# Optimization experiments

Measured on AMD Instinct MI355X. Metric: run time of the kernel, lower is better.

Reference implementation:

```python
import jax, jax.numpy as jnp
import numpy as np

BIG = 1e30  # stand-in for +inf that keeps gradients finite


def setup_inputs() -> dict:
    key = jax.random.key(0)
    B, D, N = 32, 128, 2048
    kx, ky, kl = jax.random.split(key, 3)
    x = jax.random.normal(kx, (B, D, N), dtype=jnp.float32)
    y = jax.random.normal(ky, (B, D, N), dtype=jnp.float32)
    # ragged cardinalities in [N//2, N]; every set nonempty
    lens = jax.random.randint(kl, (B,), N // 2, N + 1)
    mask = jnp.arange(N)[None, :] < lens[:, None]  # [B, N] bool
    return {"x": x, "y": y, "mask": mask}


def reference(x, y, mask):
    # x, y: [B, D, N]; mask: [B, N] bool (shared between x and y, as in original)
    xt = jnp.transpose(x, (0, 2, 1))  # [B, N, D]
    yt = jnp.transpose(y, (0, 2, 1))  # [B, N, D]
    x2 = jnp.sum(xt * xt, axis=-1)    # [B, N]
    y2 = jnp.sum(yt * yt, axis=-1)    # [B, N]
    # pairwise squared L2: [B, N, N], d[b,i,j] = ||x_i - y_j||^2
    d = x2[:, :, None] + y2[:, None, :] - 2.0 * jnp.einsum("bid,bjd->bij", xt, yt)
    m = mask
    # x_dist: for each valid y_j, min over valid x_i; then sum over valid j
    d_row = jnp.where(m[:, :, None], d, BIG)              # mask invalid i
    x_dist = jnp.sum(jnp.where(m, jnp.min(d_row, axis=1), 0.0), axis=1)  # [B]
    # y_dist: for each valid x_i, min over valid y_j; then sum over valid i
    d_col = jnp.where(m[:, None, :], d, BIG)              # mask invalid j
    y_dist = jnp.sum(jnp.where(m, jnp.min(d_col, axis=2), 0.0), axis=1)  # [B]
    return jnp.mean(x_dist + y_dist)
```

## Files before the change

kernel.cpp:

```cpp
#include <hip/hip_runtime.h>
#include <hip/hip_bf16.h>

#define BATCH 32
#define DIM   128
#define NPTS  2048
#define NCH   16
#define BIGF  1e30f

#define OFF_XT   0ull
#define OFF_YT   16777216ull
#define OFF_XN   33554432ull
#define OFF_YN   (OFF_XN + 262144ull)
#define OFF_RMIN (OFF_XN + 2ull * 262144ull)
#define OFF_CMIN (OFF_XN + 3ull * 262144ull)

typedef __bf16 bf16x8 __attribute__((ext_vector_type(8)));
typedef float  f32x16 __attribute__((ext_vector_type(16)));

#define ZERO16 {0.f,0.f,0.f,0.f,0.f,0.f,0.f,0.f,0.f,0.f,0.f,0.f,0.f,0.f,0.f,0.f}

__device__ __forceinline__ bool mask_is_i32(const void* m) {
  return ((const unsigned char*)m)[1] == 0;
}
__device__ __forceinline__ bool mask_at(const void* m, bool i32, int idx) {
  return i32 ? (((const int*)m)[idx] != 0) : (((const unsigned char*)m)[idx] != 0);
}

__global__ void chamfer_prep(const float* __restrict__ x, const float* __restrict__ y,
                             const void* __restrict__ mask, char* __restrict__ ws,
                             float* __restrict__ out) {
  __shared__ float buf[128 * 132];
  __shared__ float nrm_part[2][128];

  int blk = blockIdx.x;
  int arr = blk >> 9;
  int b   = (blk >> 4) & 31;
  int nt  = blk & 15;
  int n0  = nt << 7;
  int tid = threadIdx.x;
  bool i32m = mask_is_i32(mask);

  if (blk == 0 && tid == 0) out[0] = 0.f;

  float*    nrm  = (float*)(ws + (arr ? OFF_YN : OFF_XN));
  unsigned* cmin = (unsigned*)(ws + OFF_CMIN);

  if (!mask_at(mask, i32m, b * NPTS + n0)) {
    if (tid < 128) {
      nrm[b * NPTS + n0 + tid] = BIGF;
      if (arr) cmin[b * NPTS + n0 + tid] = __float_as_uint(BIGF);
    }
    return;
  }

  const float* src = (arr ? y : x) + (size_t)b * DIM * NPTS;
#pragma unroll
  for (int k = 0; k < 16; ++k) {
    int idx = k * 256 + tid;
    int d = idx >> 5, c4 = idx & 31;
    *(float4*)&buf[d * 132 + c4 * 4] =
        *(const float4*)(src + (size_t)d * NPTS + n0 + c4 * 4);
  }
  __syncthreads();

  int n = tid & 127, half = tid >> 7;
  char* imgbase = ws + (arr ? OFF_YT : OFF_XT);
  float sq = 0.f;
#pragma unroll
  for (int cl = 0; cl < 8; ++cl) {
    unsigned short h[8];
#pragma unroll
    for (int q = 0; q < 8; ++q) {
      float v = buf[(half * 64 + cl * 8 + q) * 132 + n];
      __hip_bfloat16 bv = __float2bfloat16(v);
      h[q] = *(unsigned short*)&bv;
      float vb = __bfloat162float(bv);
      sq = fmaf(vb, vb, sq);
    }
    uint4 pk;
    pk.x = h[0] | ((unsigned)h[1] << 16);
    pk.y = h[2] | ((unsigned)h[3] << 16);
    pk.z = h[4] | ((unsigned)h[5] << 16);
    pk.w = h[6] | ((unsigned)h[7] << 16);
    int cg = half * 8 + cl;
    *(uint4*)(imgbase + (((size_t)(b * NCH + cg) * NPTS + n0 + n) << 4)) = pk;
  }
  nrm_part[half][n] = sq;
  __syncthreads();
  if (half == 0) {
    float tot = nrm_part[0][n] + nrm_part[1][n];
    int row = n0 + n;
    bool valid = mask_at(mask, i32m, b * NPTS + row);
    nrm[b * NPTS + row] = valid ? tot : BIGF;
    if (arr) cmin[b * NPTS + row] = __float_as_uint(BIGF);
  }
}

__global__ __launch_bounds__(512, 2)
void chamfer_dist(char* __restrict__ ws, const void* __restrict__ mask) {
  __shared__ __align__(16) char ysl[2][NCH * 128 * 16];
  __shared__ unsigned colmin_lds[NPTS];
  __shared__ int lred[8];

  int blk = blockIdx.x;
  int b  = blk & 31;
  int it = blk >> 5;
  int i0 = it << 8;
  int tid = threadIdx.x, lane = tid & 63, w = tid >> 6;
  int qrow = w >> 1, qcol = w & 1, la31 = lane & 31, la5 = lane >> 5;

  bool i32m = mask_is_i32(mask);
  int cnt = 0;
#pragma unroll
  for (int k = 0; k < 4; ++k)
    cnt += mask_at(mask, i32m, b * NPTS + k * 512 + tid) ? 1 : 0;
#pragma unroll
  for (int s = 1; s < 64; s <<= 1) cnt += __shfl_xor(cnt, s);
  if (lane == 0) lred[w] = cnt;
  __syncthreads();
  int len = 0;
#pragma unroll
  for (int k = 0; k < 8; ++k) len += lred[k];
  if (i0 >= len) return;

  const char* xTb = ws + OFF_XT + ((size_t)b * NCH * NPTS << 4);
  const char* yTb = ws + OFF_YT + ((size_t)b * NCH * NPTS << 4);
  const float* xng = (const float*)(ws + OFF_XN) + b * NPTS;
  const float* yng = (const float*)(ws + OFF_YN) + b * NPTS;
  float*    rowming = (float*)(ws + OFF_RMIN) + b * NPTS;
  unsigned* colming = (unsigned*)(ws + OFF_CMIN) + b * NPTS;

#pragma unroll
  for (int k = 0; k < 4; ++k)
    colmin_lds[k * 512 + tid] = __float_as_uint(BIGF);

  int r0 = i0 + qrow * 64 + la31;
  bf16x8 Areg0[8], Areg1[8];
#pragma unroll
  for (int kc = 0; kc < 8; ++kc) {
    int c = kc * 2 + la5;
    Areg0[kc] = *(const bf16x8*)(xTb + (((size_t)c * NPTS + r0) << 4));
    Areg1[kc] = *(const bf16x8*)(xTb + (((size_t)c * NPTS + r0 + 32) << 4));
  }

  float xnr[2][16], rmin[2][16];
#pragma unroll
  for (int fm = 0; fm < 2; ++fm)
#pragma unroll
    for (int r = 0; r < 16; ++r) {
      int row = qrow * 64 + fm * 32 + (r & 3) + ((r >> 2) << 3) + (la5 << 2);
      xnr[fm][r] = xng[i0 + row];
      rmin[fm][r] = BIGF;
    }

  int nT = (len + 127) >> 7;

#pragma unroll
  for (int k = 0; k < 4; ++k) {
    int idx = k * 512 + tid;
    *(uint4*)(ysl[0] + idx * 16) =
        *(const uint4*)(yTb + (((size_t)(idx >> 7) * NPTS + (idx & 127)) << 4));
  }
  __syncthreads();

  for (int jt = 0; jt < nT; ++jt) {
    int cur = jt & 1;
    uint4 stg0, stg1, stg2, stg3;
    if (jt + 1 < nT) {
      int j0n = (jt + 1) << 7;
      int i0d = tid, i1d = 512 + tid, i2d = 1024 + tid, i3d = 1536 + tid;
      stg0 = *(const uint4*)(yTb + (((size_t)(i0d >> 7) * NPTS + j0n + (i0d & 127)) << 4));
      stg1 = *(const uint4*)(yTb + (((size_t)(i1d >> 7) * NPTS + j0n + (i1d & 127)) << 4));
      stg2 = *(const uint4*)(yTb + (((size_t)(i2d >> 7) * NPTS + j0n + (i2d & 127)) << 4));
      stg3 = *(const uint4*)(yTb + (((size_t)(i3d >> 7) * NPTS + j0n + (i3d & 127)) << 4));
    }
    int j0t = (jt << 7) + qcol * 64;
    float ynr0 = yng[j0t + la31];
    float ynr1 = yng[j0t + 32 + la31];

    const char* ybuf = (const char*)ysl[cur];
    f32x16 acc00 = ZERO16, acc01 = ZERO16, acc10 = ZERO16, acc11 = ZERO16;
#pragma unroll
    for (int kc = 0; kc < 8; ++kc) {
      int boff = ((kc * 2 + la5) * 128 + qcol * 64 + la31) << 4;
      bf16x8 b0 = *(const bf16x8*)(ybuf + boff);
      bf16x8 b1 = *(const bf16x8*)(ybuf + boff + (32 << 4));
      acc00 = __builtin_amdgcn_mfma_f32_32x32x16_bf16(Areg0[kc], b0, acc00, 0, 0, 0);
      acc01 = __builtin_amdgcn_mfma_f32_32x32x16_bf16(Areg0[kc], b1, acc01, 0, 0, 0);
      acc10 = __builtin_amdgcn_mfma_f32_32x32x16_bf16(Areg1[kc], b0, acc10, 0, 0, 0);
      acc11 = __builtin_amdgcn_mfma_f32_32x32x16_bf16(Areg1[kc], b1, acc11, 0, 0, 0);
    }
    float cm0 = BIGF, cm1 = BIGF;
#pragma unroll
    for (int r = 0; r < 16; ++r) {
      float u00 = fmaf(-2.f, acc00[r], ynr0);
      float u01 = fmaf(-2.f, acc01[r], ynr1);
      float u10 = fmaf(-2.f, acc10[r], ynr0);
      float u11 = fmaf(-2.f, acc11[r], ynr1);
      rmin[0][r] = fminf(rmin[0][r], fminf(u00, u01));
      rmin[1][r] = fminf(rmin[1][r], fminf(u10, u11));
      cm0 = fminf(cm0, fminf(u00 + xnr[0][r], u10 + xnr[1][r]));
      cm1 = fminf(cm1, fminf(u01 + xnr[0][r], u11 + xnr[1][r]));
    }
    cm0 = fminf(cm0, __shfl_xor(cm0, 32));
    cm1 = fminf(cm1, __shfl_xor(cm1, 32));
    if (lane < 32) {
      atomicMin(&colmin_lds[j0t + la31],      __float_as_uint(fmaxf(cm0, 0.f)));
      atomicMin(&colmin_lds[j0t + 32 + la31], __float_as_uint(fmaxf(cm1, 0.f)));
    }
    if (jt + 1 < nT) {
      char* dst = (char*)ysl[cur ^ 1];
      *(uint4*)(dst + (size_t)(tid)        * 16) = stg0;
      *(uint4*)(dst + (size_t)(512  + tid) * 16) = stg1;
      *(uint4*)(dst + (size_t)(1024 + tid) * 16) = stg2;
      *(uint4*)(dst + (size_t)(1536 + tid) * 16) = stg3;
    }
    __syncthreads();
  }

  int jmax = nT << 7; if (jmax > NPTS) jmax = NPTS;
  for (int idx = tid; idx < jmax; idx += 512)
    atomicMin(&colming[idx], colmin_lds[idx]);

#pragma unroll
  for (int fm = 0; fm < 2; ++fm)
#pragma unroll
    for (int r = 0; r < 16; ++r) {
      float v = rmin[fm][r];
      v = fminf(v, __shfl_xor(v, 1));
      v = fminf(v, __shfl_xor(v, 2));
      v = fminf(v, __shfl_xor(v, 4));
      v = fminf(v, __shfl_xor(v, 8));
      v = fminf(v, __shfl_xor(v, 16));
      if (la31 == 0) {
        int row = qrow * 64 + fm * 32 + (r & 3) + ((r >> 2) << 3) + (la5 << 2);
        rowming[i0 + row] = fmaxf(v + xnr[fm][r], 0.f);
      }
    }
}

__global__ void chamfer_reduce(const char* __restrict__ ws, const void* __restrict__ mask,
                               float* __restrict__ out) {
  __shared__ float red[256];
  int blk = blockIdx.x;
  int b = blk >> 2, sl = blk & 3;
  int tid = threadIdx.x;
  bool i32m = mask_is_i32(mask);
  const float*    rowmin = (const float*)(ws + OFF_RMIN) + b * NPTS;
  const unsigned* colmin = (const unsigned*)(ws + OFF_CMIN) + b * NPTS;
  float s = 0.f;
#pragma unroll
  for (int k = 0; k < 2; ++k) {
    int i = sl * 512 + k * 256 + tid;
    if (mask_at(mask, i32m, b * NPTS + i))
      s += rowmin[i] + __uint_as_float(colmin[i]);
  }
  red[tid] = s;
  __syncthreads();
  for (int st = 128; st > 0; st >>= 1) {
    if (tid < st) red[tid] += red[tid + st];
    __syncthreads();
  }
  if (tid == 0) atomicAdd(out, red[0] * (1.f / BATCH));
}

extern "C" void kernel_launch(void* const* d_in, const int* in_sizes, int n_in,
                              void* d_out, int out_size, void* d_ws, size_t ws_size,
                              hipStream_t stream) {
  const float* x = (const float*)d_in[0];
  const float* y = (const float*)d_in[1];
  const void* mask = d_in[2];
  float* out = (float*)d_out;
  char* ws = (char*)d_ws;

  chamfer_prep<<<1024, 256, 0, stream>>>(x, y, mask, ws, out);
  chamfer_dist<<<256, 512, 0, stream>>>(ws, mask);
  chamfer_reduce<<<128, 256, 0, stream>>>(ws, mask, out);
}
```

Measured before the change: 146.4 us.

## Use persistent work-queue distance kernel with smaller row tiles and direct LDS loads

Adds a tiny kernel that finds each batch's length by binary search and builds a compacted list of valid 128-row work items. The distance kernel becomes persistent: blocks pull items from an atomic counter instead of using a fixed grid where many blocks exit early. Row tiles shrink from 256 to 128 rows with one A fragment per wave, and occupancy is raised to 4 blocks per CU. Y tiles are now staged with global_load_lds rather than through registers, and the prep kernel uses 64-column tiles. The trade-offs are one extra kernel launch, more column-min atomics per row, and halved MFMA reuse per B fragment.

```diff
diff --git a/kernel.cpp b/kernel.cpp
--- a/kernel.cpp
+++ b/kernel.cpp
@@ -7,15 +7,20 @@
 #define NCH   16
 #define BIGF  1e30f
 
-#define OFF_XT   0ull
-#define OFF_YT   16777216ull
-#define OFF_XN   33554432ull
-#define OFF_YN   (OFF_XN + 262144ull)
-#define OFF_RMIN (OFF_XN + 2ull * 262144ull)
-#define OFF_CMIN (OFF_XN + 3ull * 262144ull)
+#define OFF_XT    0ull
+#define OFF_YT    16777216ull
+#define OFF_XN    33554432ull
+#define OFF_YN    (OFF_XN + 262144ull)
+#define OFF_RMIN  (OFF_XN + 2ull * 262144ull)
+#define OFF_CMIN  (OFF_XN + 3ull * 262144ull)
+#define OFF_LEN   (OFF_XN + 4ull * 262144ull)
+#define OFF_ITEMS (OFF_LEN + 128ull)
+#define OFF_CTR   (OFF_ITEMS + 2048ull)
+#define OFF_NIT   (OFF_CTR + 4ull)
 
 typedef __bf16 bf16x8 __attribute__((ext_vector_type(8)));
 typedef float  f32x16 __attribute__((ext_vector_type(16)));
+typedef unsigned int u32;
 
 #define ZERO16 {0.f,0.f,0.f,0.f,0.f,0.f,0.f,0.f,0.f,0.f,0.f,0.f,0.f,0.f,0.f,0.f}
 
@@ -24,19 +29,53 @@
 }
 __device__ __forceinline__ bool mask_at(const void* m, bool i32, int idx) {
   return i32 ? (((const int*)m)[idx] != 0) : (((const unsigned char*)m)[idx] != 0);
+}
+
+__device__ __forceinline__ void gll16(const void* g, void* l) {
+  __builtin_amdgcn_global_load_lds(
+      (const __attribute__((address_space(1))) u32*)g,
+      (__attribute__((address_space(3))) u32*)l, 16, 0, 0);
+}
+
+__global__ void chamfer_items(const void* __restrict__ mask, char* __restrict__ ws) {
+  __shared__ int cnts[32], offs[32];
+  int tid = threadIdx.x;
+  bool i32m = mask_is_i32(mask);
+  if (tid < 32) {
+    int lo = 0, hi = NPTS;
+    while (lo < hi) {
+      int mid = (lo + hi) >> 1;
+      if (mask_at(mask, i32m, tid * NPTS + mid)) lo = mid + 1; else hi = mid;
+    }
+    ((int*)(ws + OFF_LEN))[tid] = lo;
+    cnts[tid] = (lo + 127) >> 7;
+  }
+  __syncthreads();
+  if (tid == 0) {
+    int acc = 0;
+    for (int b = 0; b < 32; ++b) { offs[b] = acc; acc += cnts[b]; }
+    ((int*)(ws + OFF_NIT))[0] = acc;
+    ((int*)(ws + OFF_CTR))[0] = 0;
+  }
+  __syncthreads();
+  if (tid < 32) {
+    int o = offs[tid], c = cnts[tid];
+    int* items = (int*)(ws + OFF_ITEMS);
+    for (int k = 0; k < c; ++k) items[o + k] = (tid << 8) | k;
+  }
 }
 
 __global__ void chamfer_prep(const float* __restrict__ x, const float* __restrict__ y,
                              const void* __restrict__ mask, char* __restrict__ ws,
                              float* __restrict__ out) {
-  __shared__ float buf[128 * 132];
-  __shared__ float nrm_part[2][128];
+  __shared__ float buf[128 * 65];
+  __shared__ float nrm_part[4][64];
 
   int blk = blockIdx.x;
-  int arr = blk >> 9;
-  int b   = (blk >> 4) & 31;
-  int nt  = blk & 15;
-  int n0  = nt << 7;
+  int arr = blk >> 10;
+  int b   = (blk >> 5) & 31;
+  int nt  = blk & 31;
+  int n0  = nt << 6;
   int tid = threadIdx.x;
   bool i32m = mask_is_i32(mask);
 
@@ -46,7 +85,7 @@
   unsigned* cmin = (unsigned*)(ws + OFF_CMIN);
 
   if (!mask_at(mask, i32m, b * NPTS + n0)) {
-    if (tid < 128) {
+    if (tid < 64) {
       nrm[b * NPTS + n0 + tid] = BIGF;
       if (arr) cmin[b * NPTS + n0 + tid] = __float_as_uint(BIGF);
     }
@@ -55,23 +94,23 @@
 
   const float* src = (arr ? y : x) + (size_t)b * DIM * NPTS;
 #pragma unroll
-  for (int k = 0; k < 16; ++k) {
+  for (int k = 0; k < 8; ++k) {
     int idx = k * 256 + tid;
-    int d = idx >> 5, c4 = idx & 31;
-    *(float4*)&buf[d * 132 + c4 * 4] =
+    int d = idx >> 4, c4 = idx & 15;
+    *(float4*)&buf[d * 65 + c4 * 4] =
         *(const float4*)(src + (size_t)d * NPTS + n0 + c4 * 4);
   }
   __syncthreads();
 
-  int n = tid & 127, half = tid >> 7;
+  int n = tid & 63, grp = tid >> 6;
   char* imgbase = ws + (arr ? OFF_YT : OFF_XT);
   float sq = 0.f;
 #pragma unroll
-  for (int cl = 0; cl < 8; ++cl) {
+  for (int cl = 0; cl < 4; ++cl) {
     unsigned short h[8];
 #pragma unroll
     for (int q = 0; q < 8; ++q) {
-      float v = buf[(half * 64 + cl * 8 + q) * 132 + n];
+      float v = buf[(grp * 32 + cl * 8 + q) * 65 + n];
       __hip_bfloat16 bv = __float2bfloat16(v);
       h[q] = *(unsigned short*)&bv;
       float vb = __bfloat162float(bv);
@@ -82,13 +121,13 @@
     pk.y = h[2] | ((unsigned)h[3] << 16);
     pk.z = h[4] | ((unsigned)h[5] << 16);
     pk.w = h[6] | ((unsigned)h[7] << 16);
-    int cg = half * 8 + cl;
+    int cg = grp * 4 + cl;
     *(uint4*)(imgbase + (((size_t)(b * NCH + cg) * NPTS + n0 + n) << 4)) = pk;
   }
-  nrm_part[half][n] = sq;
-  __syncthreads();
-  if (half == 0) {
-    float tot = nrm_part[0][n] + nrm_part[1][n];
+  nrm_part[grp][n] = sq;
+  __syncthreads();
+  if (grp == 0) {
+    float tot = nrm_part[0][n] + nrm_part[1][n] + nrm_part[2][n] + nrm_part[3][n];
     int row = n0 + n;
     bool valid = mask_at(mask, i32m, b * NPTS + row);
     nrm[b * NPTS + row] = valid ? tot : BIGF;
@@ -96,147 +135,128 @@
   }
 }
 
-__global__ __launch_bounds__(512, 2)
-void chamfer_dist(char* __restrict__ ws, const void* __restrict__ mask) {
+__global__ __launch_bounds__(512, 4)
+void chamfer_dist(char* __restrict__ ws) {
   __shared__ __align__(16) char ysl[2][NCH * 128 * 16];
   __shared__ unsigned colmin_lds[NPTS];
-  __shared__ int lred[8];
-
-  int blk = blockIdx.x;
-  int b  = blk & 31;
-  int it = blk >> 5;
-  int i0 = it << 8;
+  __shared__ unsigned rowmin_lds[128];
+  __shared__ int sh_item;
+
   int tid = threadIdx.x, lane = tid & 63, w = tid >> 6;
-  int qrow = w >> 1, qcol = w & 1, la31 = lane & 31, la5 = lane >> 5;
-
-  bool i32m = mask_is_i32(mask);
-  int cnt = 0;
-#pragma unroll
-  for (int k = 0; k < 4; ++k)
-    cnt += mask_at(mask, i32m, b * NPTS + k * 512 + tid) ? 1 : 0;
-#pragma unroll
-  for (int s = 1; s < 64; s <<= 1) cnt += __shfl_xor(cnt, s);
-  if (lane == 0) lred[w] = cnt;
-  __syncthreads();
-  int len = 0;
-#pragma unroll
-  for (int k = 0; k < 8; ++k) len += lred[k];
-  if (i0 >= len) return;
-
-  const char* xTb = ws + OFF_XT + ((size_t)b * NCH * NPTS << 4);
-  const char* yTb = ws + OFF_YT + ((size_t)b * NCH * NPTS << 4);
-  const float* xng = (const float*)(ws + OFF_XN) + b * NPTS;
-  const float* yng = (const float*)(ws + OFF_YN) + b * NPTS;
-  float*    rowming = (float*)(ws + OFF_RMIN) + b * NPTS;
-  unsigned* colming = (unsigned*)(ws + OFF_CMIN) + b * NPTS;
-
-#pragma unroll
-  for (int k = 0; k < 4; ++k)
-    colmin_lds[k * 512 + tid] = __float_as_uint(BIGF);
-
-  int r0 = i0 + qrow * 64 + la31;
-  bf16x8 Areg0[8], Areg1[8];
-#pragma unroll
-  for (int kc = 0; kc < 8; ++kc) {
-    int c = kc * 2 + la5;
-    Areg0[kc] = *(const bf16x8*)(xTb + (((size_t)c * NPTS + r0) << 4));
-    Areg1[kc] = *(const bf16x8*)(xTb + (((size_t)c * NPTS + r0 + 32) << 4));
-  }
-
-  float xnr[2][16], rmin[2][16];
-#pragma unroll
-  for (int fm = 0; fm < 2; ++fm)
+  int qrow = w >> 1, qcol = w & 1;
+  int la31 = lane & 31, la5 = lane >> 5;
+
+  int* ctr = (int*)(ws + OFF_CTR);
+  const int* items = (const int*)(ws + OFF_ITEMS);
+  const int* leng  = (const int*)(ws + OFF_LEN);
+  int n_items = *(const int*)(ws + OFF_NIT);
+
+  for (;;) {
+    if (tid == 0) sh_item = atomicAdd(ctr, 1);
+    __syncthreads();
+    int ii = sh_item;
+    if (ii >= n_items) break;
+    int itm = items[ii];
+    int b = itm >> 8, i0 = (itm & 255) << 7;
+    int len = leng[b];
+    int nT = (len + 127) >> 7;
+    int jmax = nT << 7;
+
+    const char* xTb = ws + OFF_XT + ((size_t)b * NCH * NPTS << 4);
+    const char* yTb = ws + OFF_YT + ((size_t)b * NCH * NPTS << 4);
+    const float* xng = (const float*)(ws + OFF_XN) + b * NPTS;
+    const float* yng = (const float*)(ws + OFF_YN) + b * NPTS;
+    float*    rowming = (float*)(ws + OFF_RMIN) + b * NPTS;
+    unsigned* colming = (unsigned*)(ws + OFF_CMIN) + b * NPTS;
+
+    for (int idx = tid; idx < jmax; idx += 512)
+      colmin_lds[idx] = __float_as_uint(BIGF);
+    if (tid < 128) rowmin_lds[tid] = __float_as_uint(BIGF);
+
+    int r0 = i0 + qrow * 32 + la31;
+    bf16x8 Areg[8];
+#pragma unroll
+    for (int kc = 0; kc < 8; ++kc)
+      Areg[kc] = *(const bf16x8*)(xTb + (((size_t)(kc * 2 + la5) * NPTS + r0) << 4));
+
+    float xnr[16], rmin[16];
 #pragma unroll
     for (int r = 0; r < 16; ++r) {
-      int row = qrow * 64 + fm * 32 + (r & 3) + ((r >> 2) << 3) + (la5 << 2);
-      xnr[fm][r] = xng[i0 + row];
-      rmin[fm][r] = BIGF;
-    }
-
-  int nT = (len + 127) >> 7;
-
-#pragma unroll
-  for (int k = 0; k < 4; ++k) {
-    int idx = k * 512 + tid;
-    *(uint4*)(ysl[0] + idx * 16) =
-        *(const uint4*)(yTb + (((size_t)(idx >> 7) * NPTS + (idx & 127)) << 4));
-  }
-  __syncthreads();
-
-  for (int jt = 0; jt < nT; ++jt) {
-    int cur = jt & 1;
-    uint4 stg0, stg1, stg2, stg3;
-    if (jt + 1 < nT) {
-      int j0n = (jt + 1) << 7;
-      int i0d = tid, i1d = 512 + tid, i2d = 1024 + tid, i3d = 1536 + tid;
-      stg0 = *(const uint4*)(yTb + (((size_t)(i0d >> 7) * NPTS + j0n + (i0d & 127)) << 4));
-      stg1 = *(const uint4*)(yTb + (((size_t)(i1d >> 7) * NPTS + j0n + (i1d & 127)) << 4));
-      stg2 = *(const uint4*)(yTb + (((size_t)(i2d >> 7) * NPTS + j0n + (i2d & 127)) << 4));
-      stg3 = *(const uint4*)(yTb + (((size_t)(i3d >> 7) * NPTS + j0n + (i3d & 127)) << 4));
-    }
-    int j0t = (jt << 7) + qcol * 64;
-    float ynr0 = yng[j0t + la31];
-    float ynr1 = yng[j0t + 32 + la31];
-
-    const char* ybuf = (const char*)ysl[cur];
-    f32x16 acc00 = ZERO16, acc01 = ZERO16, acc10 = ZERO16, acc11 = ZERO16;
-#pragma unroll
-    for (int kc = 0; kc < 8; ++kc) {
-      int boff = ((kc * 2 + la5) * 128 + qcol * 64 + la31) << 4;
-      bf16x8 b0 = *(const bf16x8*)(ybuf + boff);
-      bf16x8 b1 = *(const bf16x8*)(ybuf + boff + (32 << 4));
-      acc00 = __builtin_amdgcn_mfma_f32_32x32x16_bf16(Areg0[kc], b0, acc00, 0, 0, 0);
-      acc01 = __builtin_amdgcn_mfma_f32_32x32x16_bf16(Areg0[kc], b1, acc01, 0, 0, 0);
-      acc10 = __builtin_amdgcn_mfma_f32_32x32x16_bf16(Areg1[kc], b0, acc10, 0, 0, 0);
-      acc11 = __builtin_amdgcn_mfma_f32_32x32x16_bf16(Areg1[kc], b1, acc11, 0, 0, 0);
-    }
-    float cm0 = BIGF, cm1 = BIGF;
+      int row_l = (r & 3) + ((r >> 2) << 3) + (la5 << 2);
+      xnr[r] = xng[i0 + qrow * 32 + row_l];
+      rmin[r] = BIGF;
+    }
+
+#pragma unroll
+    for (int k = 0; k < 4; ++k) {
+      int idx = k * 512 + tid;
+      gll16(yTb + (((size_t)(idx >> 7) * NPTS + (idx & 127)) << 4),
+            ysl[0] + idx * 16);
+    }
+    __syncthreads();
+
+    for (int jt = 0; jt < nT; ++jt) {
+      int cur = jt & 1;
+      if (jt + 1 < nT) {
+        int j0n = (jt + 1) << 7;
+#pragma unroll
+        for (int k = 0; k < 4; ++k) {
+          int idx = k * 512 + tid;
+          gll16(yTb + (((size_t)(idx >> 7) * NPTS + j0n + (idx & 127)) << 4),
+                ysl[cur ^ 1] + idx * 16);
+        }
+      }
+      int j0t = (jt << 7) + qcol * 64;
+      float ynr0 = yng[j0t + la31];
+      float ynr1 = yng[j0t + 32 + la31];
+
+      const char* ybuf = ysl[cur];
+      f32x16 acc0 = ZERO16, acc1 = ZERO16;
+#pragma unroll
+      for (int kc = 0; kc < 8; ++kc) {
+        int boff = ((kc * 2 + la5) * 128 + qcol * 64 + la31) << 4;
+        bf16x8 b0 = *(const bf16x8*)(ybuf + boff);
+        bf16x8 b1 = *(const bf16x8*)(ybuf + boff + (32 << 4));
+        acc0 = __builtin_amdgcn_mfma_f32_32x32x16_bf16(Areg[kc], b0, acc0, 0, 0, 0);
+        acc1 = __builtin_amdgcn_mfma_f32_32x32x16_bf16(Areg[kc], b1, acc1, 0, 0, 0);
+      }
+      float cm0 = BIGF, cm1 = BIGF;
+#pragma unroll
+      for (int r = 0; r < 16; ++r) {
+        float u0 = fmaf(-2.f, acc0[r], ynr0);
+        float u1 = fmaf(-2.f, acc1[r], ynr1);
+        rmin[r] = fminf(rmin[r], fminf(u0, u1));
+        cm0 = fminf(cm0, u0 + xnr[r]);
+        cm1 = fminf(cm1, u1 + xnr[r]);
+      }
+      cm0 = fminf(cm0, __shfl_xor(cm0, 32));
+      cm1 = fminf(cm1, __shfl_xor(cm1, 32));
+      if (lane < 32) {
+        atomicMin(&colmin_lds[j0t + la31],      __float_as_uint(fmaxf(cm0, 0.f)));
+        atomicMin(&colmin_lds[j0t + 32 + la31], __float_as_uint(fmaxf(cm1, 0.f)));
+      }
+      __syncthreads();
+    }
+
 #pragma unroll
     for (int r = 0; r < 16; ++r) {
-      float u00 = fmaf(-2.f, acc00[r], ynr0);
-      float u01 = fmaf(-2.f, acc01[r], ynr1);
-      float u10 = fmaf(-2.f, acc10[r], ynr0);
-      float u11 = fmaf(-2.f, acc11[r], ynr1);
-      rmin[0][r] = fminf(rmin[0][r], fminf(u00, u01));
-      rmin[1][r] = fminf(rmin[1][r], fminf(u10, u11));
-      cm0 = fminf(cm0, fminf(u00 + xnr[0][r], u10 + xnr[1][r]));
-      cm1 = fminf(cm1, fminf(u01 + xnr[0][r], u11 + xnr[1][r]));
-    }
-    cm0 = fminf(cm0, __shfl_xor(cm0, 32));
-    cm1 = fminf(cm1, __shfl_xor(cm1, 32));
-    if (lane < 32) {
-      atomicMin(&colmin_lds[j0t + la31],      __float_as_uint(fmaxf(cm0, 0.f)));
-      atomicMin(&colmin_lds[j0t + 32 + la31], __float_as_uint(fmaxf(cm1, 0.f)));
-    }
-    if (jt + 1 < nT) {
-      char* dst = (char*)ysl[cur ^ 1];
-      *(uint4*)(dst + (size_t)(tid)        * 16) = stg0;
-      *(uint4*)(dst + (size_t)(512  + tid) * 16) = stg1;
-      *(uint4*)(dst + (size_t)(1024 + tid) * 16) = stg2;
-      *(uint4*)(dst + (size_t)(1536 + tid) * 16) = stg3;
-    }
-    __syncthreads();
-  }
-
-  int jmax = nT << 7; if (jmax > NPTS) jmax = NPTS;
-  for (int idx = tid; idx < jmax; idx += 512)
-    atomicMin(&colming[idx], colmin_lds[idx]);
-
-#pragma unroll
-  for (int fm = 0; fm < 2; ++fm)
-#pragma unroll
-    for (int r = 0; r < 16; ++r) {
-      float v = rmin[fm][r];
+      float v = rmin[r];
       v = fminf(v, __shfl_xor(v, 1));
       v = fminf(v, __shfl_xor(v, 2));
       v = fminf(v, __shfl_xor(v, 4));
       v = fminf(v, __shfl_xor(v, 8));
       v = fminf(v, __shfl_xor(v, 16));
       if (la31 == 0) {
-        int row = qrow * 64 + fm * 32 + (r & 3) + ((r >> 2) << 3) + (la5 << 2);
-        rowming[i0 + row] = fmaxf(v + xnr[fm][r], 0.f);
-      }
-    }
+        int row_l = qrow * 32 + (r & 3) + ((r >> 2) << 3) + (la5 << 2);
+        atomicMin(&rowmin_lds[row_l], __float_as_uint(fmaxf(v + xnr[r], 0.f)));
+      }
+    }
+    __syncthreads();
+    if (tid < 128) rowming[i0 + tid] = __uint_as_float(rowmin_lds[tid]);
+    for (int idx = tid; idx < jmax; idx += 512)
+      atomicMin(&colming[idx], colmin_lds[idx]);
+    __syncthreads();
+  }
 }
 
 __global__ void chamfer_reduce(const char* __restrict__ ws, const void* __restrict__ mask,
@@ -273,7 +293,8 @@
   float* out = (float*)d_out;
   char* ws = (char*)d_ws;
 
-  chamfer_prep<<<1024, 256, 0, stream>>>(x, y, mask, ws, out);
-  chamfer_dist<<<256, 512, 0, stream>>>(ws, mask);
+  chamfer_items<<<1, 64, 0, stream>>>(mask, ws);
+  chamfer_prep<<<2048, 256, 0, stream>>>(x, y, mask, ws, out);
+  chamfer_dist<<<512, 512, 0, stream>>>(ws);
   chamfer_reduce<<<128, 256, 0, stream>>>(ws, mask, out);
 }
```

Result: slower. 160.2 us (+9.5%).
